# Performance work log

Measured on AMD Instinct MI355X. Metric: run time of the kernel, lower is better.

Reference implementation:

```python
import jax, jax.numpy as jnp
import numpy as np

GN_EPS = 1e-5
NN_EPS = 1e-8


def _three_nn_interpolate(xyz1, xyz2, points2):
    # xyz1: (B,N,3), xyz2: (B,M,3), points2: (B,M,C) -> (B,N,C)
    src_sq = jnp.sum(xyz1 ** 2, axis=-1, keepdims=True)          # (B,N,1)
    dst_sq = jnp.sum(xyz2 ** 2, axis=-1)[:, None, :]             # (B,1,M)
    inner = jnp.einsum('bnd,bmd->bnm', xyz1, xyz2)               # (B,N,M)
    dist = src_sq - 2.0 * inner + dst_sq                         # (B,N,M)
    neg_d, idx = jax.lax.top_k(-dist, 3)                         # (B,N,3)
    d = -neg_d
    inv = 1.0 / (d + NN_EPS)
    w = inv / jnp.sum(inv, axis=-1, keepdims=True)               # (B,N,3)
    grouped = jax.vmap(lambda p, i: p[i])(points2, idx)          # (B,N,3,C)
    return jnp.sum(grouped * w[..., None], axis=2)               # (B,N,C)


def _group_norm(x, weight, bias, groups):
    # x: (B,C,N)
    B, C, N = x.shape
    xg = x.reshape(B, groups, C // groups, N)
    mu = jnp.mean(xg, axis=(2, 3), keepdims=True)
    var = jnp.var(xg, axis=(2, 3), keepdims=True)
    xg = (xg - mu) * jax.lax.rsqrt(var + GN_EPS)
    x = xg.reshape(B, C, N)
    return x * weight[None, :, None] + bias[None, :, None]


def setup_inputs() -> dict:
    key = jax.random.key(0)
    ks = jax.random.split(key, 10)
    B, N, M, C1, C2 = 8, 8192, 2048, 128, 256
    mlp = [256, 128]
    in_ch = C1 + C2
    inp = {
        'xyz1': jax.random.normal(ks[0], (B, N, 3), dtype=jnp.float32),
        'xyz2': jax.random.normal(ks[1], (B, M, 3), dtype=jnp.float32),
        'points1': jax.random.normal(ks[2], (B, N, C1), dtype=jnp.float32),
        'points2': jax.random.normal(ks[3], (B, M, C2), dtype=jnp.float32),
        'w0': jax.random.normal(ks[4], (mlp[0], in_ch), dtype=jnp.float32) * (1.0 / np.sqrt(in_ch)),
        'w1': jax.random.normal(ks[5], (mlp[1], mlp[0]), dtype=jnp.float32) * (1.0 / np.sqrt(mlp[0])),
        'gn0_w': jnp.ones((mlp[0],), dtype=jnp.float32),
        'gn0_b': jnp.zeros((mlp[0],), dtype=jnp.float32),
        'gn1_w': jnp.ones((mlp[1],), dtype=jnp.float32),
        'gn1_b': jnp.zeros((mlp[1],), dtype=jnp.float32),
    }
    return inp


def reference(xyz1, xyz2, points1, points2, w0, w1, gn0_w, gn0_b, gn1_w, gn1_b):
    interpolated = _three_nn_interpolate(xyz1, xyz2, points2)    # (B,N,C2)
    feat = jnp.concatenate([points1, interpolated], axis=-1)     # (B,N,C1+C2)
    # conv1d kernel size 1 == pointwise matmul; work in (B,C,N) layout for GN
    h = jnp.einsum('bnc,oc->bon', feat, w0)                      # (B,256,N)
    h = jax.nn.relu(_group_norm(h, gn0_w, gn0_b, groups=min(32, w0.shape[0])))
    h = jnp.einsum('bcn,oc->bon', h, w1)                         # (B,128,N)
    h = jax.nn.relu(_group_norm(h, gn1_w, gn1_b, groups=min(32, w1.shape[0])))
    return jnp.transpose(h, (0, 2, 1))                           # (B,N,128)
```

## Files before the change

### kernel.cpp

```cpp
#include <hip/hip_runtime.h>


#define DEVI __device__ __forceinline__

static constexpr int B  = 8;
static constexpr int N  = 8192;
static constexpr int M  = 2048;
static constexpr int C1 = 128;
static constexpr int C2 = 256;
static constexpr int CIN = C1 + C2;
static constexpr int H0 = 256;
static constexpr int H1 = 128;
static constexpr int BN = B * N;
static constexpr int NSEG = 8;
static constexpr int SEGL = M / NSEG;
static constexpr int SL = 64;

typedef __bf16 bf16x8 __attribute__((ext_vector_type(8)));
typedef float  f32x4  __attribute__((ext_vector_type(4)));
typedef unsigned short ushort8v __attribute__((ext_vector_type(8)));

DEVI float bf2f(unsigned short u) {
    union { unsigned int i; float f; } v; v.i = ((unsigned int)u) << 16; return v.f;
}
DEVI unsigned short f2bf(float f) {
    union { float f; unsigned int i; } v; v.f = f;
    unsigned int x = v.i;
    return (unsigned short)((x + 0x7fffu + ((x >> 16) & 1u)) >> 16);
}
DEVI float ldin(const void* p, size_t i, int bf) {
    return bf ? bf2f(((const unsigned short*)p)[i]) : ((const float*)p)[i];
}
DEVI void ld8(const void* p, size_t i, int bf, float r[8]) {
    if (bf) {
        const ushort8v u = *(const ushort8v*)((const unsigned short*)p + i);
#pragma unroll
        for (int k = 0; k < 8; k++) r[k] = bf2f(u[k]);
    } else {
        const float4 a = *(const float4*)((const float*)p + i);
        const float4 b = *(const float4*)((const float*)p + i + 4);
        r[0] = a.x; r[1] = a.y; r[2] = a.z; r[3] = a.w;
        r[4] = b.x; r[5] = b.y; r[6] = b.z; r[7] = b.w;
    }
}

DEVI void gload16(const void* g, void* l) {
    __builtin_amdgcn_global_load_lds(
        (const __attribute__((address_space(1))) void*)g,
        (__attribute__((address_space(3))) void*)l, 16, 0, 0);
}

__global__ __launch_bounds__(64) void detect_dtype_kernel(const void* __restrict__ xyz1,
                                                          int* __restrict__ flag)
{
    const unsigned short* u = (const unsigned short*)xyz1;
    const int lane = threadIdx.x;
    const float av = fabsf(bf2f(u[2 * lane]));
    const bool in_range = (av >= 1e-4f && av <= 100.0f);
    const unsigned long long m = __ballot(in_range);
    if (lane == 0) flag[0] = (__popcll(m) >= 32) ? 1 : 0;
}

__global__ __launch_bounds__(256) void prep_kernel(
    const void* __restrict__ w0, const void* __restrict__ w1,
    const void* __restrict__ xyz2,
    unsigned short* __restrict__ w0b, unsigned short* __restrict__ w1b,
    float4* __restrict__ c4, const int* __restrict__ flag)
{
    const int bf = flag[0];
    const int n0 = H0 * CIN;
    const int n1 = H1 * H0;
    const int n2 = B * M;
    const int total = n0 + n1 + n2;
    for (int i = blockIdx.x * blockDim.x + threadIdx.x; i < total; i += gridDim.x * blockDim.x) {
        if (i < n0) {
            w0b[i] = bf ? ((const unsigned short*)w0)[i] : f2bf(((const float*)w0)[i]);
        } else if (i < n0 + n1) {
            const int j = i - n0;
            w1b[j] = bf ? ((const unsigned short*)w1)[j] : f2bf(((const float*)w1)[j]);
        } else {
            const int j = i - n0 - n1;
            const float x = ldin(xyz2, (size_t)j * 3 + 0, bf);
            const float y = ldin(xyz2, (size_t)j * 3 + 1, bf);
            const float z = ldin(xyz2, (size_t)j * 3 + 2, bf);
            const float sq = __fadd_rn(__fadd_rn(__fmul_rn(x, x), __fmul_rn(y, y)), __fmul_rn(z, z));
            c4[j] = make_float4(x, y, z, sq);
        }
    }
}

__global__ __launch_bounds__(256) void knn3_split_kernel(
    const void* __restrict__ xyz1, const float4* __restrict__ c4,
    float* __restrict__ cd, int* __restrict__ ci, const int* __restrict__ flag)
{
    const int bf = flag[0];
    const int tid = threadIdx.x;
    const int gid = blockIdx.x * 256 + tid;
    const int s = blockIdx.y;
    const int b = __builtin_amdgcn_readfirstlane(gid >> 13);

    const float x1 = ldin(xyz1, (size_t)gid * 3 + 0, bf);
    const float y1 = ldin(xyz1, (size_t)gid * 3 + 1, bf);
    const float z1 = ldin(xyz1, (size_t)gid * 3 + 2, bf);
    const float sq1 = __fadd_rn(__fadd_rn(__fmul_rn(x1, x1), __fmul_rn(y1, y1)), __fmul_rn(z1, z1));

    const float4* __restrict__ cand = c4 + b * M + s * SEGL;
    const int jbase = s * SEGL;

    float b0 = 3.4e38f, b1 = 3.4e38f, b2 = 3.4e38f;
    int   i0 = 0, i1 = 0, i2 = 0;

#pragma unroll 4
    for (int j = 0; j < SEGL; ++j) {
        const float4 p = cand[j];
        const float inner = __fadd_rn(__fadd_rn(__fmul_rn(x1, p.x), __fmul_rn(y1, p.y)),
                                      __fmul_rn(z1, p.z));
        const float d = __fadd_rn(__fsub_rn(sq1, __fmul_rn(2.0f, inner)), p.w);
        const int j2 = jbase + j;
        if (d < b2) {
            if (d < b0)      { b2 = b1; i2 = i1; b1 = b0; i1 = i0; b0 = d; i0 = j2; }
            else if (d < b1) { b2 = b1; i2 = i1; b1 = d;  i1 = j2; }
            else             { b2 = d;  i2 = j2; }
        }
    }

    const size_t base = (size_t)gid * (3 * NSEG) + s * 3;
    cd[base + 0] = b0; cd[base + 1] = b1; cd[base + 2] = b2;
    ci[base + 0] = i0; ci[base + 1] = i1; ci[base + 2] = i2;
}

__global__ __launch_bounds__(256) void knn3_merge_kernel(
    const float* __restrict__ cd, const int* __restrict__ ci,
    int* __restrict__ nn_idx, float* __restrict__ nn_w)
{
    const int gid = blockIdx.x * 256 + threadIdx.x;
    const float* d24 = cd + (size_t)gid * (3 * NSEG);
    const int*   i24 = ci + (size_t)gid * (3 * NSEG);

    float bd0 = 3.4e38f, bd1 = 3.4e38f, bd2 = 3.4e38f;
    int   bi0 = 0x7fffffff, bi1 = 0x7fffffff, bi2 = 0x7fffffff;

#pragma unroll
    for (int k = 0; k < 3 * NSEG; ++k) {
        const float d  = d24[k];
        const int   ix = i24[k];
        const bool lt2 = (d < bd2) || (d == bd2 && ix < bi2);
        if (lt2) {
            const bool lt0 = (d < bd0) || (d == bd0 && ix < bi0);
            const bool lt1 = (d < bd1) || (d == bd1 && ix < bi1);
            if (lt0)      { bd2 = bd1; bi2 = bi1; bd1 = bd0; bi1 = bi0; bd0 = d; bi0 = ix; }
            else if (lt1) { bd2 = bd1; bi2 = bi1; bd1 = d; bi1 = ix; }
            else          { bd2 = d; bi2 = ix; }
        }
    }

    const float v0 = 1.0f / (bd0 + 1e-8f);
    const float v1 = 1.0f / (bd1 + 1e-8f);
    const float v2 = 1.0f / (bd2 + 1e-8f);
    const float s = v0 + v1 + v2;
    nn_idx[gid * 3 + 0] = bi0; nn_idx[gid * 3 + 1] = bi1; nn_idx[gid * 3 + 2] = bi2;
    nn_w[gid * 3 + 0] = v0 / s; nn_w[gid * 3 + 1] = v1 / s; nn_w[gid * 3 + 2] = v2 / s;
}

__global__ __launch_bounds__(256) void interp_concat_kernel(
    const void* __restrict__ p1, const void* __restrict__ p2,
    const int* __restrict__ nn_idx, const float* __restrict__ nn_w,
    unsigned short* __restrict__ feat, const int* __restrict__ flag)
{
    const int bf = flag[0];
    const int total = BN * (CIN / 8);
    for (int idx = blockIdx.x * blockDim.x + threadIdx.x; idx < total; idx += gridDim.x * blockDim.x) {
        const int c8 = idx % 48;
        const int p  = idx / 48;
        const int c  = c8 * 8;
        float r[8];
        if (c < C1) {
            ld8(p1, (size_t)p * C1 + c, bf, r);
        } else {
            const int b  = p >> 13;
            const int c2 = c - C1;
            const int*   id = nn_idx + p * 3;
            const float* wv = nn_w  + p * 3;
            float t0[8], t1[8], t2[8];
            ld8(p2, (size_t)(b * M + id[0]) * C2 + c2, bf, t0);
            ld8(p2, (size_t)(b * M + id[1]) * C2 + c2, bf, t1);
            ld8(p2, (size_t)(b * M + id[2]) * C2 + c2, bf, t2);
            const float w0v = wv[0], w1v = wv[1], w2v = wv[2];
#pragma unroll
            for (int k = 0; k < 8; k++) r[k] = w0v * t0[k] + w1v * t1[k] + w2v * t2[k];
        }
        ushort8v o;
#pragma unroll
        for (int k = 0; k < 8; k++) o[k] = f2bf(r[k]);
        *(ushort8v*)(feat + (size_t)idx * 8) = o;
    }
}

template<int K, int COUT>
__global__ __launch_bounds__(256) void gemm_mfma_kernel(
    const unsigned short* __restrict__ A,
    const unsigned short* __restrict__ W,
    unsigned short* __restrict__ Cmat)
{
    __shared__ __align__(16) char lds[32768];

    const int tid = threadIdx.x;
    const int l   = tid & 63;
    const int w   = tid >> 6;
    const int rowBase = blockIdx.x * 128;
    const int colBase = blockIdx.y * 128;

    const int srow  = l >> 3;
    const int sslot = l & 7;

    f32x4 acc[4][4];
#pragma unroll
    for (int i = 0; i < 4; i++)
#pragma unroll
        for (int j = 0; j < 4; j++) acc[i][j] = (f32x4)0.0f;

    const int wr  = (tid >> 7) & 1;
    const int wc  = (tid >> 6) & 1;
    const int rl  = l & 15;
    const int kq  = l >> 4;
    const int swz = (l & 7) << 4;
    int aoff[4], boff[4];
#pragma unroll
    for (int i = 0; i < 4; i++) {
        aoff[i] = (wr * 64 + i * 16 + rl) * 128;
        boff[i] = 16384 + (wc * 64 + i * 16 + rl) * 128;
    }

    constexpr int NT = K / 64;

#pragma unroll 1
    for (int t = 0; t < NT; ++t) {
        {
            const int k0 = t * 64;
#pragma unroll
            for (int i = 0; i < 4; ++i) {
                const int ch = w * 4 + i;
                const int r  = ch * 8 + srow;
                const int ke = (sslot ^ (r & 7)) << 3;
                gload16(A + ((size_t)(rowBase + r) * K + k0 + ke), lds + ch * 1024);
                gload16(W + ((size_t)(colBase + r) * K + k0 + ke), lds + 16384 + ch * 1024);
            }
        }
        __syncthreads();
#pragma unroll
        for (int ks = 0; ks < 2; ++ks) {
            const int kb = (ks * 64 + kq * 16) ^ swz;
            bf16x8 af[4], bfr[4];
#pragma unroll
            for (int i = 0; i < 4; i++) af[i]  = *(const bf16x8*)(lds + aoff[i] + kb);
#pragma unroll
            for (int j = 0; j < 4; j++) bfr[j] = *(const bf16x8*)(lds + boff[j] + kb);
#pragma unroll
            for (int i = 0; i < 4; i++)
#pragma unroll
                for (int j = 0; j < 4; j++)
                    acc[i][j] = __builtin_amdgcn_mfma_f32_16x16x32_bf16(af[i], bfr[j], acc[i][j], 0, 0, 0);
        }
        __syncthreads();
    }

    const int crow = rowBase + wr * 64 + kq * 4;
    const int ccol = colBase + wc * 64 + rl;
#pragma unroll
    for (int i = 0; i < 4; i++)
#pragma unroll
        for (int j = 0; j < 4; j++)
#pragma unroll
            for (int r = 0; r < 4; r++)
                Cmat[(size_t)(crow + i * 16 + r) * COUT + ccol + j * 16] = f2bf(acc[i][j][r]);
}

__global__ __launch_bounds__(256) void gn_stats_part_kernel(
    const unsigned short* __restrict__ h, float2* __restrict__ part, int C)
{
    const int cpg = C >> 5;
    const int b  = blockIdx.x / SL;
    const int sl = blockIdx.x % SL;
    const int g  = threadIdx.x & 31;
    const int rs = threadIdx.x >> 5;
    const int rows = N / SL;

    float s = 0.f, ss = 0.f;
    for (int n = sl * rows + rs; n < (sl + 1) * rows; n += 8) {
        const unsigned short* row = h + (size_t)(b * N + n) * C + g * cpg;
        for (int c = 0; c < cpg; c += 4) {
            const ushort4 v = *(const ushort4*)(row + c);
            const float f0 = bf2f(v.x), f1 = bf2f(v.y), f2 = bf2f(v.z), f3 = bf2f(v.w);
            s  += f0 + f1 + f2 + f3;
            ss += f0 * f0 + f1 * f1 + f2 * f2 + f3 * f3;
        }
    }
    __shared__ float2 red[256];
    red[threadIdx.x] = make_float2(s, ss);
    __syncthreads();
    if (threadIdx.x < 32) {
        float2 a = red[threadIdx.x];
#pragma unroll
        for (int k = 1; k < 8; k++) {
            const float2 p = red[threadIdx.x + 32 * k];
            a.x += p.x; a.y += p.y;
        }
        part[(size_t)blockIdx.x * 32 + g] = a;
    }
}

__global__ __launch_bounds__(256) void gn_finalize_kernel(
    const float2* __restrict__ part, float2* __restrict__ st, int C)
{
    const int t = threadIdx.x;
    const int b = t >> 5;
    const int g = t & 31;
    const int cpg = C >> 5;
    float s = 0.f, ss = 0.f;
    for (int k = 0; k < SL; k++) {
        const float2 p = part[(size_t)(b * SL + k) * 32 + g];
        s += p.x; ss += p.y;
    }
    const float cnt = (float)N * (float)cpg;
    const float mu  = s / cnt;
    const float var = ss / cnt - mu * mu;
    st[t] = make_float2(mu, rsqrtf(var + 1e-5f));
}

__global__ __launch_bounds__(256) void gn_norm_relu_kernel(
    const unsigned short* __restrict__ h, const float2* __restrict__ st,
    const void* __restrict__ gw, const void* __restrict__ gb,
    void* __restrict__ out, int C, int cpg, int total4,
    const int* __restrict__ flag, int final_out)
{
    const int bf = flag[0];
    const int C4 = C >> 2;
    for (int i4 = blockIdx.x * blockDim.x + threadIdx.x; i4 < total4; i4 += gridDim.x * blockDim.x) {
        const int c = (i4 % C4) * 4;
        const int p = i4 / C4;
        const int b = p >> 13;
        const float2 ms = st[b * (C / cpg) + c / cpg];
        const ushort4 hv = *(const ushort4*)(h + (size_t)i4 * 4);
        float r[4] = { bf2f(hv.x), bf2f(hv.y), bf2f(hv.z), bf2f(hv.w) };
#pragma unroll
        for (int k = 0; k < 4; k++) {
            const float gwv = ldin(gw, c + k, bf);
            const float gbv = ldin(gb, c + k, bf);
            r[k] = fmaxf((r[k] - ms.x) * ms.y * gwv + gbv, 0.f);
        }
        if (!final_out || bf) {
            ushort4 o;
            o.x = f2bf(r[0]); o.y = f2bf(r[1]); o.z = f2bf(r[2]); o.w = f2bf(r[3]);
            *(ushort4*)((unsigned short*)out + (size_t)i4 * 4) = o;
        } else {
            float4 o; o.x = r[0]; o.y = r[1]; o.z = r[2]; o.w = r[3];
            *(float4*)((float*)out + (size_t)i4 * 4) = o;
        }
    }
}

extern "C" void kernel_launch(void* const* d_in, const int* in_sizes, int n_in,
                              void* d_out, int out_size, void* d_ws, size_t ws_size,
                              hipStream_t stream)
{
    const void* xyz1    = d_in[0];
    const void* xyz2    = d_in[1];
    const void* points1 = d_in[2];
    const void* points2 = d_in[3];
    const void* w0      = d_in[4];
    const void* w1      = d_in[5];
    const void* gn0w    = d_in[6];
    const void* gn0b    = d_in[7];
    const void* gn1w    = d_in[8];
    const void* gn1b    = d_in[9];

    char* ws = (char*)d_ws;
    int*            nn_idx = (int*)ws;
    float*          nn_w   = (float*)(ws + 786432);
    unsigned short* feat   = (unsigned short*)(ws + 1572864);
    unsigned short* h0     = (unsigned short*)(ws + 51904512);
    unsigned short* h0n    = feat;
    unsigned short* h1     = h0;
    unsigned short* w0b    = (unsigned short*)(ws + 85458944);
    unsigned short* w1b    = (unsigned short*)(ws + 85655552);
    float2*         st0    = (float2*)(ws + 85721088);
    float2*         st1    = (float2*)(ws + 85723136);
    int*            flag   = (int*)(ws + 85725184);
    float4*         c4     = (float4*)(ws + 85725248);
    float*          cd     = (float*)(ws + 85987392);
    int*            ci     = (int*)(ws + 92278848);
    float2*         part   = (float2*)(ws + 98570304);

    detect_dtype_kernel<<<1, 64, 0, stream>>>(xyz1, flag);

    prep_kernel<<<576, 256, 0, stream>>>(w0, w1, xyz2, w0b, w1b, c4, flag);

    {
        dim3 g(BN / 256, NSEG);
        knn3_split_kernel<<<g, 256, 0, stream>>>(xyz1, c4, cd, ci, flag);
    }
    knn3_merge_kernel<<<BN / 256, 256, 0, stream>>>(cd, ci, nn_idx, nn_w);

    interp_concat_kernel<<<2048, 256, 0, stream>>>(points1, points2, nn_idx, nn_w, feat, flag);

    {
        dim3 g(BN / 128, H0 / 128);
        gemm_mfma_kernel<CIN, H0><<<g, 256, 0, stream>>>(feat, w0b, h0);
    }

    gn_stats_part_kernel<<<B * SL, 256, 0, stream>>>(h0, part, H0);
    gn_finalize_kernel<<<1, 256, 0, stream>>>(part, st0, H0);
    gn_norm_relu_kernel<<<2048, 256, 0, stream>>>(h0, st0, gn0w, gn0b, (void*)h0n,
                                                  H0, H0 / 32, BN * H0 / 4, flag, 0);

    {
        dim3 g(BN / 128, H1 / 128);
        gemm_mfma_kernel<H0, H1><<<g, 256, 0, stream>>>(h0n, w1b, h1);
    }

    gn_stats_part_kernel<<<B * SL, 256, 0, stream>>>(h1, part, H1);
    gn_finalize_kernel<<<1, 256, 0, stream>>>(part, st1, H1);
    gn_norm_relu_kernel<<<1024, 256, 0, stream>>>(h1, st1, gn1w, gn1b, d_out,
                                                  H1, H1 / 32, BN * H1 / 4, flag, 1);
}
```

Before: 346.0 us.

## Use reduced FMA score with branchless top-3 in kNN split, recompute distances in merge

The split kernel now ranks candidates by a reduced score, 0.5*|p|^2 - x·p, computed with three FMAs, dropping the per-point squared norm and the factor of two. The top-3 insertion becomes a branchless min/max/select network to avoid divergent branches. Only indices are written, in a coalesced plane-major layout, and the merge kernel recomputes exact distances by gathering the 24 candidate points. This removes the distance buffer and its traffic at the cost of extra gathers in the merge, and FMA rounding may rank near-ties differently from the reference.

```diff
diff --git a/kernel.cpp b/kernel.cpp
--- a/kernel.cpp
+++ b/kernel.cpp
@@ -84,14 +84,14 @@
             const float y = ldin(xyz2, (size_t)j * 3 + 1, bf);
             const float z = ldin(xyz2, (size_t)j * 3 + 2, bf);
             const float sq = __fadd_rn(__fadd_rn(__fmul_rn(x, x), __fmul_rn(y, y)), __fmul_rn(z, z));
-            c4[j] = make_float4(x, y, z, sq);
+            c4[j] = make_float4(x, y, z, 0.5f * sq);
         }
     }
 }
 
 __global__ __launch_bounds__(256) void knn3_split_kernel(
     const void* __restrict__ xyz1, const float4* __restrict__ c4,
-    float* __restrict__ cd, int* __restrict__ ci, const int* __restrict__ flag)
+    int* __restrict__ ci, const int* __restrict__ flag)
 {
     const int bf = flag[0];
     const int tid = threadIdx.x;
@@ -102,7 +102,6 @@
     const float x1 = ldin(xyz1, (size_t)gid * 3 + 0, bf);
     const float y1 = ldin(xyz1, (size_t)gid * 3 + 1, bf);
     const float z1 = ldin(xyz1, (size_t)gid * 3 + 2, bf);
-    const float sq1 = __fadd_rn(__fadd_rn(__fmul_rn(x1, x1), __fmul_rn(y1, y1)), __fmul_rn(z1, z1));
 
     const float4* __restrict__ cand = c4 + b * M + s * SEGL;
     const int jbase = s * SEGL;
@@ -113,37 +112,56 @@
 #pragma unroll 4
     for (int j = 0; j < SEGL; ++j) {
         const float4 p = cand[j];
+        const float sc = __builtin_fmaf(-x1, p.x,
+                          __builtin_fmaf(-y1, p.y,
+                           __builtin_fmaf(-z1, p.z, p.w)));
+        const int jn = jbase + j;
+        const bool c0 = sc < b0;
+        const float t1 = fmaxf(sc, b0);
+        b0 = fminf(sc, b0);
+        const int  tj1 = c0 ? i0 : jn;
+        i0 = c0 ? jn : i0;
+        const bool c1 = t1 < b1;
+        const float t2 = fmaxf(t1, b1);
+        b1 = fminf(t1, b1);
+        const int  tj2 = c1 ? i1 : tj1;
+        i1 = c1 ? tj1 : i1;
+        const bool c2 = t2 < b2;
+        b2 = fminf(t2, b2);
+        i2 = c2 ? tj2 : i2;
+    }
+
+    ci[(size_t)(s * 3 + 0) * BN + gid] = i0;
+    ci[(size_t)(s * 3 + 1) * BN + gid] = i1;
+    ci[(size_t)(s * 3 + 2) * BN + gid] = i2;
+}
+
+__global__ __launch_bounds__(256) void knn3_merge_kernel(
+    const void* __restrict__ xyz1, const float4* __restrict__ c4,
+    const int* __restrict__ ci,
+    int* __restrict__ nn_idx, float* __restrict__ nn_w,
+    const int* __restrict__ flag)
+{
+    const int bf = flag[0];
+    const int gid = blockIdx.x * 256 + threadIdx.x;
+    const int b = gid >> 13;
+
+    const float x1 = ldin(xyz1, (size_t)gid * 3 + 0, bf);
+    const float y1 = ldin(xyz1, (size_t)gid * 3 + 1, bf);
+    const float z1 = ldin(xyz1, (size_t)gid * 3 + 2, bf);
+    const float sq1 = __fadd_rn(__fadd_rn(__fmul_rn(x1, x1), __fmul_rn(y1, y1)), __fmul_rn(z1, z1));
+
+    float bd0 = 3.4e38f, bd1 = 3.4e38f, bd2 = 3.4e38f;
+    int   bi0 = 0x7fffffff, bi1 = 0x7fffffff, bi2 = 0x7fffffff;
+
+#pragma unroll
+    for (int k = 0; k < 3 * NSEG; ++k) {
+        const int ix = ci[(size_t)k * BN + gid];
+        const float4 p = c4[b * M + ix];
         const float inner = __fadd_rn(__fadd_rn(__fmul_rn(x1, p.x), __fmul_rn(y1, p.y)),
                                       __fmul_rn(z1, p.z));
-        const float d = __fadd_rn(__fsub_rn(sq1, __fmul_rn(2.0f, inner)), p.w);
-        const int j2 = jbase + j;
-        if (d < b2) {
-            if (d < b0)      { b2 = b1; i2 = i1; b1 = b0; i1 = i0; b0 = d; i0 = j2; }
-            else if (d < b1) { b2 = b1; i2 = i1; b1 = d;  i1 = j2; }
-            else             { b2 = d;  i2 = j2; }
-        }
-    }
-
-    const size_t base = (size_t)gid * (3 * NSEG) + s * 3;
-    cd[base + 0] = b0; cd[base + 1] = b1; cd[base + 2] = b2;
-    ci[base + 0] = i0; ci[base + 1] = i1; ci[base + 2] = i2;
-}
-
-__global__ __launch_bounds__(256) void knn3_merge_kernel(
-    const float* __restrict__ cd, const int* __restrict__ ci,
-    int* __restrict__ nn_idx, float* __restrict__ nn_w)
-{
-    const int gid = blockIdx.x * 256 + threadIdx.x;
-    const float* d24 = cd + (size_t)gid * (3 * NSEG);
-    const int*   i24 = ci + (size_t)gid * (3 * NSEG);
-
-    float bd0 = 3.4e38f, bd1 = 3.4e38f, bd2 = 3.4e38f;
-    int   bi0 = 0x7fffffff, bi1 = 0x7fffffff, bi2 = 0x7fffffff;
-
-#pragma unroll
-    for (int k = 0; k < 3 * NSEG; ++k) {
-        const float d  = d24[k];
-        const int   ix = i24[k];
+        const float pw2 = p.w + p.w;
+        const float d = __fadd_rn(__fsub_rn(sq1, __fmul_rn(2.0f, inner)), pw2);
         const bool lt2 = (d < bd2) || (d == bd2 && ix < bi2);
         if (lt2) {
             const bool lt0 = (d < bd0) || (d == bd0 && ix < bi0);
@@ -387,9 +405,8 @@
     float2*         st1    = (float2*)(ws + 85723136);
     int*            flag   = (int*)(ws + 85725184);
     float4*         c4     = (float4*)(ws + 85725248);
-    float*          cd     = (float*)(ws + 85987392);
-    int*            ci     = (int*)(ws + 92278848);
-    float2*         part   = (float2*)(ws + 98570304);
+    int*            ci     = (int*)(ws + 85987392);
+    float2*         part   = (float2*)(ws + 92278848);
 
     detect_dtype_kernel<<<1, 64, 0, stream>>>(xyz1, flag);
 
@@ -397,9 +414,9 @@
 
     {
         dim3 g(BN / 256, NSEG);
-        knn3_split_kernel<<<g, 256, 0, stream>>>(xyz1, c4, cd, ci, flag);
-    }
-    knn3_merge_kernel<<<BN / 256, 256, 0, stream>>>(cd, ci, nn_idx, nn_w);
+        knn3_split_kernel<<<g, 256, 0, stream>>>(xyz1, c4, ci, flag);
+    }
+    knn3_merge_kernel<<<BN / 256, 256, 0, stream>>>(xyz1, c4, ci, nn_idx, nn_w, flag);
 
     interp_concat_kernel<<<2048, 256, 0, stream>>>(points1, points2, nn_idx, nn_w, feat, flag);
 
```

Measured after the change: 331.7 us. 4.1% less time.
